# Optimization experiments

Hardware: AMD Instinct MI355X
Metric: run time of the kernel (lower is better)

The kernel has to match this reference:

```python
import jax, jax.numpy as jnp
import numpy as np

B, H, E = 16384, 4096, 64
TEMPERATURE = 1.0
SPARSITY = 0.8
K = max(1, int(E * (1.0 - SPARSITY)))  # = 12


def setup_inputs() -> dict:
    key = jax.random.key(0)
    k1, k2, k3, k4, k5 = jax.random.split(key, 5)
    std = 0.02
    return {
        "hidden_states": jax.random.normal(k1, (B, H), dtype=jnp.float32),
        "router_w": jax.random.normal(k2, (E, H), dtype=jnp.float32) * std,
        "sparsity_mask": jax.random.normal(k3, (E, H), dtype=jnp.float32) * std,
        "gate_w1": jax.random.normal(k4, (H // 2, H), dtype=jnp.float32) * std,
        "gate_b1": jnp.zeros((H // 2,), dtype=jnp.float32),
        "gate_w2": jax.random.normal(k5, (E, H // 2), dtype=jnp.float32) * std,
        "gate_b2": jnp.zeros((E,), dtype=jnp.float32),
    }


def reference(hidden_states, router_w, sparsity_mask, gate_w1, gate_b1, gate_w2, gate_b2):
    # gate network: Linear -> ReLU -> Linear -> Sigmoid
    h = jax.nn.relu(hidden_states @ gate_w1.T + gate_b1)          # [B, H/2]
    gates = jax.nn.sigmoid(h @ gate_w2.T + gate_b2)                # [B, E]
    # masked router projection
    masked_w = router_w * jax.nn.sigmoid(sparsity_mask)            # [E, H]
    router_logits = hidden_states @ masked_w.T                     # [B, E]
    scaled_logits = (router_logits * gates) / TEMPERATURE          # [B, E]
    # top-k selection + dual softmax
    top_k_logits, top_k_indices = jax.lax.top_k(scaled_logits, K)  # [B, K]
    expert_weights = jax.nn.softmax(top_k_logits, axis=-1)         # [B, K]
    probs = jax.nn.softmax(scaled_logits, axis=-1)                 # [B, E]
    # load-balancing stats
    expert_load = probs.mean(axis=0)                               # [E]
    load_variance = jnp.var(expert_load, ddof=1)                   # torch .var() is unbiased
    entropy = -(probs * jnp.log(probs + 1e-8)).sum(axis=-1).mean()
    return scaled_logits, top_k_indices, expert_weights, load_variance, entropy
```

## Files before the change

### kernel.cpp

```cpp
#include <hip/hip_runtime.h>

#define BROWS 16384
#define HDIM  4096
#define H2    2048
#define EEXP  64
#define KSEL  12

typedef float f32x4 __attribute__((ext_vector_type(4)));

typedef __attribute__((address_space(1))) const unsigned int guint_t;
typedef __attribute__((address_space(3))) unsigned int luint_t;

__device__ __forceinline__ void gl16(const void* g, void* l){
  __builtin_amdgcn_global_load_lds((guint_t*)g, (luint_t*)l, 16, 0, 0);
}

__global__ void k_mw32(const float* __restrict__ rw, const float* __restrict__ mk,
                       float* __restrict__ mw, int n){
  int i = blockIdx.x*blockDim.x + threadIdx.x;
  if (i < n){
    float m = mk[i];
    float u = (float)exp(-(double)m);
    mw[i] = rw[i] * (1.0f/(1.0f + u));
  }
}

__global__ __launch_bounds__(256)
void k_tr(const float* __restrict__ in, float* __restrict__ out, int R, int C){
  __shared__ float tile[32][33];
  const int t = threadIdx.x;
  const int cb = C >> 5;
  const int bx = blockIdx.x % cb, by = blockIdx.x / cb;
  const int lr = t >> 3, lc4 = (t & 7) * 4;
  f32x4 v = *(const f32x4*)(in + (size_t)(by*32 + lr)*C + bx*32 + lc4);
  tile[lr][lc4] = v[0]; tile[lr][lc4+1] = v[1];
  tile[lr][lc4+2] = v[2]; tile[lr][lc4+3] = v[3];
  __syncthreads();
  f32x4 o;
  o[0] = tile[lc4][lr]; o[1] = tile[lc4+1][lr];
  o[2] = tile[lc4+2][lr]; o[3] = tile[lc4+3][lr];
  *(f32x4*)(out + (size_t)(bx*32 + lr)*R + by*32 + lc4) = o;
}

__global__ __launch_bounds__(256, 2)
void k_h(const float* __restrict__ A, const float* __restrict__ Btr,
         const float* __restrict__ bias, float* __restrict__ C)
{
  __shared__ float As[32][256];
  __shared__ float Bs[33][128];
  const int t = threadIdx.x, w = t>>6, l = t&63;
  const int ly = l>>3, lx = l&7;
  const int bid = blockIdx.x;
  const int q = bid >> 3;
  const int mt = (bid & 7)*8 + (q >> 4), nt = q & 15;
  const long m0 = (long)mt*256; const int n0 = nt*128;
  const int r0 = (w>>1)*64 + ly*8;
  const int c0 = (w&1)*64 + lx*8;

  float acc[16][8] = {};

  const int rg = t>>2, kc = (t&3)*8;
  const float* ag = A + (m0 + rg*4)*(size_t)HDIM + kc;
  f32x4 ar[4][2];
  auto loadA = [&](int kb){
    #pragma unroll
    for (int r=0;r<4;r++){
      ar[r][0] = *(const f32x4*)(ag + (size_t)r*HDIM + kb);
      ar[r][1] = *(const f32x4*)(ag + (size_t)r*HDIM + kb + 4);
    }
  };
  auto storeA = [&](){
    #pragma unroll
    for (int u=0;u<2;u++)
      #pragma unroll
      for (int v=0;v<4;v++){
        f32x4 w4;
        w4[0]=ar[0][u][v]; w4[1]=ar[1][u][v]; w4[2]=ar[2][u][v]; w4[3]=ar[3][u][v];
        *(f32x4*)&As[kc + u*4 + v][rg*4] = w4;
      }
  };
  const float* bg = Btr + n0 + (size_t)(l&31)*4 + (size_t)(l>>5)*H2;

  auto LDK = [&](int K, f32x4&A0, f32x4&A1, f32x4&A2, f32x4&A3, f32x4&B0, f32x4&B1){
    A0 = *(const f32x4*)&As[K][r0];     A1 = *(const f32x4*)&As[K][r0+4];
    A2 = *(const f32x4*)&As[K][r0+128]; A3 = *(const f32x4*)&As[K][r0+132];
    B0 = *(const f32x4*)&Bs[K][c0];     B1 = *(const f32x4*)&Bs[K][c0+4];
  };
  auto FMK = [&](const f32x4&A0, const f32x4&A1, const f32x4&A2, const f32x4&A3,
                 const f32x4&B0, const f32x4&B1){
    #pragma unroll
    for (int i=0;i<4;i++)
      #pragma unroll
      for (int j=0;j<4;j++){
        acc[i][j]      = fmaf(A0[i], B0[j], acc[i][j]);
        acc[i][j+4]    = fmaf(A0[i], B1[j], acc[i][j+4]);
        acc[i+4][j]    = fmaf(A1[i], B0[j], acc[i+4][j]);
        acc[i+4][j+4]  = fmaf(A1[i], B1[j], acc[i+4][j+4]);
        acc[i+8][j]    = fmaf(A2[i], B0[j], acc[i+8][j]);
        acc[i+8][j+4]  = fmaf(A2[i], B1[j], acc[i+8][j+4]);
        acc[i+12][j]   = fmaf(A3[i], B0[j], acc[i+12][j]);
        acc[i+12][j+4] = fmaf(A3[i], B1[j], acc[i+12][j+4]);
      }
  };

  for (int p = 0; p < 128; ++p){
    loadA(p*32);
    __syncthreads();
    {
      const size_t kro = (size_t)(p*32 + w*8)*H2;
      #pragma unroll
      for (int i=0;i<4;i++)
        gl16(bg + kro + (size_t)(2*i)*H2, &Bs[w*8 + 2*i][0]);
    }
    storeA();
    asm volatile("s_waitcnt vmcnt(0)" ::: "memory");
    __syncthreads();

    f32x4 xa0,xa1,xa2,xa3,xb0,xb1, ya0,ya1,ya2,ya3,yb0,yb1;
    LDK(0, xa0,xa1,xa2,xa3,xb0,xb1);
    #pragma unroll 2
    for (int kk = 0; kk < 32; kk += 2){
      LDK(kk+1, ya0,ya1,ya2,ya3,yb0,yb1);
      FMK(xa0,xa1,xa2,xa3,xb0,xb1);
      LDK(kk+2, xa0,xa1,xa2,xa3,xb0,xb1);
      FMK(ya0,ya1,ya2,ya3,yb0,yb1);
    }
  }

  const float* bp = bias + n0 + c0;
  f32x4 bv0 = *(const f32x4*)bp, bv1 = *(const f32x4*)(bp+4);
  #pragma unroll
  for (int i=0;i<16;i++){
    const long row = m0 + r0 + ((i<8) ? i : (128 + i - 8));
    f32x4 v0, v1;
    #pragma unroll
    for (int j=0;j<4;j++){
      v0[j] = fmaxf(acc[i][j]   + bv0[j], 0.f);
      v1[j] = fmaxf(acc[i][j+4] + bv1[j], 0.f);
    }
    *(f32x4*)&C[row*(long)H2 + n0 + c0]     = v0;
    *(f32x4*)&C[row*(long)H2 + n0 + c0 + 4] = v1;
  }
}

__global__ __launch_bounds__(256, 2)
void k_g32(const float* __restrict__ A, const float* __restrict__ B,
           float* __restrict__ C, int K, int ntiles,
           const float* __restrict__ bias, int relu)
{
  __shared__ float As[64][36];
  __shared__ float Bs[64][36];
  const int t = threadIdx.x;
  const int mt = blockIdx.x / ntiles, nt = blockIdx.x % ntiles;
  const long m0 = (long)mt*64; const int n0 = nt*64;
  const int ty = t>>4, tx = t&15;
  const int sr = t>>2, sc = (t&3)*8;
  float acc[4][4] = {{0.f,0.f,0.f,0.f},{0.f,0.f,0.f,0.f},
                     {0.f,0.f,0.f,0.f},{0.f,0.f,0.f,0.f}};
  const float* ap = A + (m0+sr)*(long)K + sc;
  const float* bp = B + ((size_t)(n0+sr))*K + sc;
  f32x4 a0,a1,b0,b1;
  auto gload = [&](int kb){
    a0 = *(const f32x4*)(ap + kb);
    a1 = *(const f32x4*)(ap + kb + 4);
    b0 = *(const f32x4*)(bp + kb);
    b1 = *(const f32x4*)(bp + kb + 4);
  };
  gload(0);
  for (int kb = 0; kb < K; kb += 32){
    __syncthreads();
    *(f32x4*)&As[sr][sc]   = a0; *(f32x4*)&As[sr][sc+4] = a1;
    *(f32x4*)&Bs[sr][sc]   = b0; *(f32x4*)&Bs[sr][sc+4] = b1;
    __syncthreads();
    if (kb + 32 < K) gload(kb + 32);
    #pragma unroll
    for (int kk = 0; kk < 32; kk += 4){
      f32x4 av[4], bv[4];
      #pragma unroll
      for (int i=0;i<4;i++) av[i] = *(const f32x4*)&As[ty+16*i][kk];
      #pragma unroll
      for (int j=0;j<4;j++) bv[j] = *(const f32x4*)&Bs[tx+16*j][kk];
      #pragma unroll
      for (int q=0;q<4;q++)
        #pragma unroll
        for (int i=0;i<4;i++)
          #pragma unroll
          for (int j=0;j<4;j++)
            acc[i][j] = fmaf(av[i][q], bv[j][q], acc[i][j]);
    }
  }
  #pragma unroll
  for (int i=0;i<4;i++){
    const long row = m0 + ty + 16*i;
    #pragma unroll
    for (int j=0;j<4;j++){
      const int col = n0 + tx + 16*j;
      float v = acc[i][j];
      if (bias) v = v + bias[col];
      if (relu) v = fmaxf(v, 0.f);
      C[row*(long)(ntiles*64) + col] = v;
    }
  }
}

__global__ void k_sig(const float* __restrict__ z, const float* __restrict__ rl,
                      const float* __restrict__ b2, float* __restrict__ s,
                      float* __restrict__ out0, int n){
  int i = blockIdx.x*blockDim.x + threadIdx.x;
  if (i < n){
    int e = i & (EEXP-1);
    float zz = z[i] + b2[e];
    float u = (float)exp(-(double)zz);
    float g = 1.0f/(1.0f + u);
    float sv = rl[i] * g;
    s[i] = sv;
    out0[i] = sv;
  }
}

__global__ __launch_bounds__(256, 2)
void k_top(const float* __restrict__ s32, float* __restrict__ out,
           float* __restrict__ loadp, float* __restrict__ entp)
{
  __shared__ float P[256][65];
  __shared__ float entbuf[256];
  const int t = threadIdx.x;
  const long row = (long)blockIdx.x*256 + t;
  const float* srow = s32 + row*EEXP;

  float vals[KSEL]; int idxs[KSEL];
  float pv = INFINITY; int pi = -1;
  for (int kk=0; kk<KSEL; ++kk){
    float bv = -INFINITY; int bi = 0;
    for (int e=0; e<EEXP; ++e){
      float v = srow[e];
      bool after = (v < pv) || ((v == pv) && (e > pi));
      if (after && (v > bv)){ bv = v; bi = e; }
    }
    vals[kk] = bv; idxs[kk] = bi; pv = bv; pi = bi;
  }
  float* oi = out + (size_t)BROWS*EEXP;
  float* ow = oi + (size_t)BROWS*KSEL;
  const long obase = row*KSEL;
  {
    float ev[KSEL]; float sw = 0.f;
    #pragma unroll
    for (int kk=0; kk<KSEL; ++kk){ ev[kk] = expf(vals[kk]-vals[0]); sw += ev[kk]; }
    float inv = 1.f/sw;
    #pragma unroll
    for (int kk=0; kk<KSEL; ++kk){ oi[obase+kk] = (float)idxs[kk]; ow[obase+kk] = ev[kk]*inv; }
  }
  {
    float mx = vals[0];
    float sum = 0.f;
    for (int e=0; e<EEXP; ++e) sum += expf(srow[e] - mx);
    float isum = 1.f/sum, ent = 0.f;
    for (int e=0; e<EEXP; ++e){
      float p2 = expf(srow[e] - mx) * isum;
      ent -= p2 * logf(p2 + 1e-8f);
      P[t][e] = p2;
    }
    entbuf[t] = ent;
  }
  __syncthreads();
  if (t < 64){
    float s = 0.f;
    for (int r2=0; r2<256; ++r2) s += P[r2][t];
    loadp[blockIdx.x*64 + t] = s;
    float es = entbuf[t] + entbuf[t+64] + entbuf[t+128] + entbuf[t+192];
    for (int o=32; o; o>>=1) es += __shfl_down(es, o);
    if (t == 0) entp[blockIdx.x] = es;
  }
}

__global__ void k_finalize(const float* __restrict__ loadp, const float* __restrict__ entp,
                           float* __restrict__ out){
  const int e = threadIdx.x;
  float s = 0.f;
  for (int b=0; b<64; ++b) s += loadp[b*64 + e];
  float load = s * (1.f/16384.f);
  float tsum = load;
  for (int o=32; o; o>>=1) tsum += __shfl_xor(tsum, o);
  float mean = tsum * (1.f/64.f);
  float d = load - mean;
  float v = d*d;
  for (int o=32; o; o>>=1) v += __shfl_xor(v, o);
  float var = v * (1.f/63.f);
  float es = entp[e];
  for (int o=32; o; o>>=1) es += __shfl_xor(es, o);
  if (e == 0){
    size_t off = (size_t)BROWS*EEXP + (size_t)BROWS*KSEL*2;
    out[off]     = var;
    out[off + 1] = es * (1.f/16384.f);
  }
}

extern "C" void kernel_launch(void* const* d_in, const int* in_sizes, int n_in,
                              void* d_out, int out_size, void* d_ws, size_t ws_size,
                              hipStream_t stream)
{
  const float* hidden = (const float*)d_in[0];
  const float* rw     = (const float*)d_in[1];
  const float* mk     = (const float*)d_in[2];
  const float* gw1    = (const float*)d_in[3];
  const float* gb1    = (const float*)d_in[4];
  const float* gw2    = (const float*)d_in[5];
  const float* gb2    = (const float*)d_in[6];
  float* out = (float*)d_out;

  unsigned char* ws = (unsigned char*)d_ws;
  size_t o = 0;
  float* mw  = (float*)(ws + o); o += (size_t)EEXP*HDIM*4;
  float* Btr = (float*)(ws + o); o += (size_t)HDIM*H2*4;
  float* h   = (float*)(ws + o); o += (size_t)BROWS*H2*4;
  float* rl  = (float*)(ws + o); o += (size_t)BROWS*EEXP*4;
  float* zb  = (float*)(ws + o); o += (size_t)BROWS*EEXP*4;
  float* s32 = (float*)(ws + o); o += (size_t)BROWS*EEXP*4;
  float* loadp = (float*)(ws + o); o += 64*64*4;
  float* entp  = (float*)(ws + o); o += 256;

  k_mw32<<<(EEXP*HDIM+255)/256, 256, 0, stream>>>(rw, mk, mw, EEXP*HDIM);
  k_tr<<<(HDIM/32)*(H2/32), 256, 0, stream>>>(gw1, Btr, H2, HDIM);
  k_h<<<(BROWS/256)*(H2/128), 256, 0, stream>>>(hidden, Btr, gb1, h);
  k_g32<<<(BROWS/64)*1, 256, 0, stream>>>(hidden, mw, rl, HDIM, 1, nullptr, 0);
  k_g32<<<(BROWS/64)*1, 256, 0, stream>>>(h, gw2, zb, H2, 1, nullptr, 0);
  k_sig<<<(BROWS*EEXP+255)/256, 256, 0, stream>>>(zb, rl, gb2, s32, out, BROWS*EEXP);
  k_top<<<BROWS/256, 256, 0, stream>>>(s32, out, loadp, entp);
  k_finalize<<<1, 64, 0, stream>>>(loadp, entp, out);
}
```

Baseline: 3.665 ms.

## Double-buffer A/B tiles in gate GEMM to overlap loads with FMA

Restructures the hidden-layer GEMM main loop to use two LDS buffers with a K-step of 16 instead of a single 32-deep buffer. The next tile's B DMA and A global loads are issued before computing the current tile, so memory latency overlaps the FMA work, and only one barrier is needed per step. The A tile row stride is padded to 260 to reduce LDS bank conflicts. The cost is twice as many loop iterations and barriers, plus the A prefetch registers being held across compute, which raises register pressure.

```diff
diff --git a/kernel.cpp b/kernel.cpp
--- a/kernel.cpp
+++ b/kernel.cpp
@@ -5,6 +5,7 @@
 #define H2    2048
 #define EEXP  64
 #define KSEL  12
+#define KP    16
 
 typedef float f32x4 __attribute__((ext_vector_type(4)));
 
@@ -46,8 +47,8 @@
 void k_h(const float* __restrict__ A, const float* __restrict__ Btr,
          const float* __restrict__ bias, float* __restrict__ C)
 {
-  __shared__ float As[32][256];
-  __shared__ float Bs[33][128];
+  __shared__ float As[2][KP][260];
+  __shared__ float Bs[2][KP][128];
   const int t = threadIdx.x, w = t>>6, l = t&63;
   const int ly = l>>3, lx = l&7;
   const int bid = blockIdx.x;
@@ -59,72 +60,70 @@
 
   float acc[16][8] = {};
 
-  const int rg = t>>2, kc = (t&3)*8;
-  const float* ag = A + (m0 + rg*4)*(size_t)HDIM + kc;
-  f32x4 ar[4][2];
-  auto loadA = [&](int kb){
-    #pragma unroll
-    for (int r=0;r<4;r++){
-      ar[r][0] = *(const f32x4*)(ag + (size_t)r*HDIM + kb);
-      ar[r][1] = *(const f32x4*)(ag + (size_t)r*HDIM + kb + 4);
-    }
-  };
-  auto storeA = [&](){
-    #pragma unroll
-    for (int u=0;u<2;u++)
-      #pragma unroll
-      for (int v=0;v<4;v++){
-        f32x4 w4;
-        w4[0]=ar[0][u][v]; w4[1]=ar[1][u][v]; w4[2]=ar[2][u][v]; w4[3]=ar[3][u][v];
-        *(f32x4*)&As[kc + u*4 + v][rg*4] = w4;
-      }
-  };
-  const float* bg = Btr + n0 + (size_t)(l&31)*4 + (size_t)(l>>5)*H2;
-
-  auto LDK = [&](int K, f32x4&A0, f32x4&A1, f32x4&A2, f32x4&A3, f32x4&B0, f32x4&B1){
-    A0 = *(const f32x4*)&As[K][r0];     A1 = *(const f32x4*)&As[K][r0+4];
-    A2 = *(const f32x4*)&As[K][r0+128]; A3 = *(const f32x4*)&As[K][r0+132];
-    B0 = *(const f32x4*)&Bs[K][c0];     B1 = *(const f32x4*)&Bs[K][c0+4];
-  };
-  auto FMK = [&](const f32x4&A0, const f32x4&A1, const f32x4&A2, const f32x4&A3,
-                 const f32x4&B0, const f32x4&B1){
-    #pragma unroll
-    for (int i=0;i<4;i++)
-      #pragma unroll
-      for (int j=0;j<4;j++){
-        acc[i][j]      = fmaf(A0[i], B0[j], acc[i][j]);
-        acc[i][j+4]    = fmaf(A0[i], B1[j], acc[i][j+4]);
-        acc[i+4][j]    = fmaf(A1[i], B0[j], acc[i+4][j]);
-        acc[i+4][j+4]  = fmaf(A1[i], B1[j], acc[i+4][j+4]);
-        acc[i+8][j]    = fmaf(A2[i], B0[j], acc[i+8][j]);
-        acc[i+8][j+4]  = fmaf(A2[i], B1[j], acc[i+8][j+4]);
-        acc[i+12][j]   = fmaf(A3[i], B0[j], acc[i+12][j]);
-        acc[i+12][j+4] = fmaf(A3[i], B1[j], acc[i+12][j+4]);
-      }
-  };
-
-  for (int p = 0; p < 128; ++p){
-    loadA(p*32);
-    __syncthreads();
-    {
-      const size_t kro = (size_t)(p*32 + w*8)*H2;
+  const int rg = t & 63, kq = t >> 6;
+  const float* ag = A + (m0 + rg*4)*(size_t)HDIM + kq*4;
+  f32x4 ar[4];
+  auto loadA = [&](int p){
+    #pragma unroll
+    for (int r=0;r<4;r++)
+      ar[r] = *(const f32x4*)(ag + (size_t)r*HDIM + p*KP);
+  };
+  auto storeA = [&](int buf){
+    #pragma unroll
+    for (int j=0;j<4;j++){
+      f32x4 w4;
+      w4[0]=ar[0][j]; w4[1]=ar[1][j]; w4[2]=ar[2][j]; w4[3]=ar[3][j];
+      *(f32x4*)&As[buf][kq*4 + j][rg*4] = w4;
+    }
+  };
+  const float* bg = Btr + n0 + (size_t)(l>>5)*H2 + (size_t)(l&31)*4;
+  auto dmaB = [&](int p, int buf){
+    #pragma unroll
+    for (int i=0;i<2;i++)
+      gl16(bg + (size_t)(p*KP + w*4 + 2*i)*H2, &Bs[buf][w*4 + 2*i][0]);
+  };
+
+  auto compute = [&](int buf){
+    #pragma unroll 4
+    for (int kk = 0; kk < KP; ++kk){
+      f32x4 A0 = *(const f32x4*)&As[buf][kk][r0];
+      f32x4 A1 = *(const f32x4*)&As[buf][kk][r0+4];
+      f32x4 A2 = *(const f32x4*)&As[buf][kk][r0+128];
+      f32x4 A3 = *(const f32x4*)&As[buf][kk][r0+132];
+      f32x4 B0 = *(const f32x4*)&Bs[buf][kk][c0];
+      f32x4 B1 = *(const f32x4*)&Bs[buf][kk][c0+4];
       #pragma unroll
       for (int i=0;i<4;i++)
-        gl16(bg + kro + (size_t)(2*i)*H2, &Bs[w*8 + 2*i][0]);
-    }
-    storeA();
+        #pragma unroll
+        for (int j=0;j<4;j++){
+          acc[i][j]      = fmaf(A0[i], B0[j], acc[i][j]);
+          acc[i][j+4]    = fmaf(A0[i], B1[j], acc[i][j+4]);
+          acc[i+4][j]    = fmaf(A1[i], B0[j], acc[i+4][j]);
+          acc[i+4][j+4]  = fmaf(A1[i], B1[j], acc[i+4][j+4]);
+          acc[i+8][j]    = fmaf(A2[i], B0[j], acc[i+8][j]);
+          acc[i+8][j+4]  = fmaf(A2[i], B1[j], acc[i+8][j+4]);
+          acc[i+12][j]   = fmaf(A3[i], B0[j], acc[i+12][j]);
+          acc[i+12][j+4] = fmaf(A3[i], B1[j], acc[i+12][j+4]);
+        }
+    }
+  };
+
+  loadA(0);
+  storeA(0);
+  dmaB(0, 0);
+  asm volatile("s_waitcnt vmcnt(0)" ::: "memory");
+  __syncthreads();
+
+  for (int p = 0; p < HDIM/KP; ++p){
+    const int buf = p & 1;
+    if (p < HDIM/KP - 1){
+      dmaB(p+1, buf^1);
+      loadA(p+1);
+    }
+    compute(buf);
+    if (p < HDIM/KP - 1) storeA(buf^1);
     asm volatile("s_waitcnt vmcnt(0)" ::: "memory");
     __syncthreads();
-
-    f32x4 xa0,xa1,xa2,xa3,xb0,xb1, ya0,ya1,ya2,ya3,yb0,yb1;
-    LDK(0, xa0,xa1,xa2,xa3,xb0,xb1);
-    #pragma unroll 2
-    for (int kk = 0; kk < 32; kk += 2){
-      LDK(kk+1, ya0,ya1,ya2,ya3,yb0,yb1);
-      FMK(xa0,xa1,xa2,xa3,xb0,xb1);
-      LDK(kk+2, xa0,xa1,xa2,xa3,xb0,xb1);
-      FMK(ya0,ya1,ya2,ya3,yb0,yb1);
-    }
   }
 
   const float* bp = bias + n0 + c0;
```

New measurement: 3.706 ms. About the same (+1.1%).
